# Kernel optimization log

Hardware: AMD Instinct MI355X
Metric: run time of the kernel (lower is better)

The kernel has to match this reference:

```python
import jax, jax.numpy as jnp
import numpy as np

N_NODES = 100000
N_EDGES = 3200000
BN_EPS = 1e-5


def setup_inputs() -> dict:
    key = jax.random.key(0)
    ks = jax.random.split(key, 16)
    return {
        "x": jax.random.normal(ks[0], (N_NODES, 2), jnp.float32),
        "eq_labels": jax.random.randint(ks[1], (N_NODES,), 0, 32, jnp.int32),
        "edge_index": jax.random.randint(ks[2], (2, N_EDGES), 0, N_NODES, jnp.int32),
        "eq_emb": jax.random.normal(ks[3], (32, 8), jnp.float32),
        "W1_0": jax.random.normal(ks[4], (10, 64), jnp.float32) * 0.3,
        "b1_0": jnp.zeros((64,), jnp.float32),
        "W2_0": jax.random.normal(ks[5], (64, 64), jnp.float32) * 0.12,
        "b2_0": jnp.zeros((64,), jnp.float32),
        "eps_0": jnp.zeros((), jnp.float32),
        "gamma_0": jnp.ones((64,), jnp.float32),
        "beta_0": jnp.zeros((64,), jnp.float32),
        "W1_s": jax.random.normal(ks[6], (2, 64, 64), jnp.float32) * 0.12,
        "b1_s": jnp.zeros((2, 64), jnp.float32),
        "W2_s": jax.random.normal(ks[7], (2, 64, 64), jnp.float32) * 0.12,
        "b2_s": jnp.zeros((2, 64), jnp.float32),
        "eps_s": jnp.zeros((2,), jnp.float32),
        "gamma_s": jnp.ones((2, 64), jnp.float32),
        "beta_s": jnp.zeros((2, 64), jnp.float32),
        "Wf": jax.random.normal(ks[8], (64, 1), jnp.float32) * 0.12,
        "bf": jnp.zeros((1,), jnp.float32),
    }


def _gin_bn_relu(h, src, dst, W1, b1, W2, b2, eps, gamma, beta):
    # GINConv: (1+eps)*x_i + sum_{j->i} x_j, then 2-layer ReLU MLP, then BN, ReLU
    agg = jax.ops.segment_sum(h[src], dst, num_segments=N_NODES)
    h = (1.0 + eps) * h + agg
    h = jax.nn.relu(h @ W1 + b1)
    h = jax.nn.relu(h @ W2 + b2)
    mu = jnp.mean(h, axis=0)
    var = jnp.var(h, axis=0)
    h = (h - mu) * jax.lax.rsqrt(var + BN_EPS) * gamma + beta
    return jax.nn.relu(h)


def reference(x, eq_labels, edge_index, eq_emb, W1_0, b1_0, W2_0, b2_0, eps_0,
              gamma_0, beta_0, W1_s, b1_s, W2_s, b2_s, eps_s, gamma_s, beta_s,
              Wf, bf):
    src, dst = edge_index[0], edge_index[1]
    h = jnp.concatenate([x, eq_emb[eq_labels]], axis=-1)  # [N, 10]
    h = _gin_bn_relu(h, src, dst, W1_0, b1_0, W2_0, b2_0, eps_0, gamma_0, beta_0)
    for i in range(2):
        h = _gin_bn_relu(h, src, dst, W1_s[i], b1_s[i], W2_s[i], b2_s[i],
                         eps_s[i], gamma_s[i], beta_s[i])
    return (h @ Wf + bf).squeeze(-1)  # [N]
```

## Files before the change

### kernel.cpp

```cpp
#include <hip/hip_runtime.h>

#define N_NODES 100000
#define N_EDGES 3200000
#define BN_EPS 1e-5f

#define BLK_NODES 128
#define NBLK 782
#define CHUNK 16384
#define NW ((N_EDGES + CHUNK - 1) / CHUNK)
#define BCAP 4480
#define CUR_PAD 16
#define NSLICE 32

typedef unsigned int uint;
typedef unsigned short ushort;
typedef _Float16 half_t;
typedef __attribute__((ext_vector_type(8))) _Float16 h8v;
typedef __attribute__((ext_vector_type(4))) float f4v;

__device__ inline float bf_lo(uint u) { return __uint_as_float(u << 16); }
__device__ inline float bf_hi(uint u) { return __uint_as_float(u & 0xffff0000u); }
__device__ inline float h_lo(uint u) {
    union { ushort s; half_t h; } r; r.s = (ushort)(u & 0xffffu); return (float)r.h;
}
__device__ inline float h_hi(uint u) {
    union { ushort s; half_t h; } r; r.s = (ushort)(u >> 16); return (float)r.h;
}
__device__ inline ushort f2bf(float a) {
    uint ua = __float_as_uint(a); ua += 0x7fffu + ((ua >> 16) & 1u);
    return (ushort)(ua >> 16);
}
__device__ inline ushort f2h(float a) {
    union { half_t h; ushort u; } r;
    r.h = (half_t)a;
    return r.u;
}
__device__ inline uint packh2(float a, float b) {
    return (uint)f2h(a) | ((uint)f2h(b) << 16);
}
__device__ inline h8v loadH(const ushort* p) {
    union { uint4 q; h8v f; } r;
    r.q = *(const uint4*)p;
    return r.f;
}
__device__ inline h8v loadHh(const half_t* p) {
    union { uint4 q; h8v f; } r;
    r.q = *(const uint4*)p;
    return r.f;
}
__device__ inline f4v mfma16(h8v a, h8v b, f4v c) {
    return __builtin_amdgcn_mfma_f32_16x16x32_f16(a, b, c, 0, 0, 0);
}

#define FETCH_COLS(rr, st, dg, mx, wv, wv2)                                   \
    {                                                                         \
        int _r = (rr);                                                        \
        st = __shfl(myStart, 2 * _r + hl, 64);                                \
        dg = __shfl(myDeg, 2 * _r + hl, 64);                                  \
        int _dA = __shfl(myDeg, 2 * _r, 64);                                  \
        int _dB = __shfl(myDeg, 2 * _r + 1, 64);                              \
        mx = max(_dA, _dB);                                                   \
        int _e1 = min(l5, dg - 1); _e1 = _e1 < 0 ? 0 : _e1;                   \
        int _e2 = min(32 + l5, dg - 1); _e2 = _e2 < 0 ? 0 : _e2;              \
        wv = col[st + _e1];                                                   \
        wv2 = col[st + _e2];                                                  \
    }

__global__ __launch_bounds__(256) void k_h0(const float* __restrict__ x,
                                            const int* __restrict__ lab,
                                            const float* __restrict__ emb,
                                            ushort* __restrict__ h0,
                                            const float* __restrict__ W1_0,
                                            const float* __restrict__ W2_0,
                                            const float* __restrict__ W1_s,
                                            const float* __restrict__ W2_s,
                                            ushort* __restrict__ W0t,
                                            ushort* __restrict__ W20t,
                                            ushort* __restrict__ Wst, int n) {
    int i = blockIdx.x * blockDim.x + threadIdx.x;
    if (i < n) {
        float v[16];
        v[0] = x[2 * i];
        v[1] = x[2 * i + 1];
        int L = lab[i];
#pragma unroll
        for (int k = 0; k < 8; k++) v[2 + k] = emb[L * 8 + k];
#pragma unroll
        for (int k = 10; k < 16; k++) v[k] = 0.f;
        uint o8[8];
#pragma unroll
        for (int k = 0; k < 8; k++) o8[k] = packh2(v[2 * k], v[2 * k + 1]);
        uint4* o = (uint4*)(h0 + (size_t)i * 16);
        o[0] = uint4{o8[0], o8[1], o8[2], o8[3]};
        o[1] = uint4{o8[4], o8[5], o8[6], o8[7]};
    }
    if (blockIdx.x == 0) {
        int t = threadIdx.x;
        for (int j = t; j < 64 * 32; j += 256) {
            int nn = j >> 5, k = j & 31;
            W0t[j] = (k < 10) ? f2h(W1_0[k * 64 + nn]) : (ushort)0;
        }
        for (int j = t; j < 4096; j += 256) {
            int nn = j >> 6, k = j & 63;
            W20t[j] = f2h(W2_0[k * 64 + nn]);
        }
        for (int l = 0; l < 2; l++) {
            const float* w1 = W1_s + l * 4096;
            const float* w2 = W2_s + l * 4096;
            for (int j = t; j < 4096; j += 256) {
                int nn = j >> 6, k = j & 63;
                Wst[l * 8192 + j] = f2h(w1[k * 64 + nn]);
                Wst[l * 8192 + 4096 + j] = f2h(w2[k * 64 + nn]);
            }
        }
    }
}

__global__ __launch_bounds__(256) void k_fill(const int* __restrict__ src,
                                              const int* __restrict__ dst,
                                              int* __restrict__ gcur,
                                              int* __restrict__ bucket) {
    __shared__ int cnt[NBLK];
    __shared__ int off[NBLK];
    int t = threadIdx.x;
    for (int b = t; b < NBLK; b += 256) cnt[b] = 0;
    __syncthreads();
    int my0 = blockIdx.x * CHUNK + t * 64;
    for (int k = 0; k < 64; k += 4) {
        int e = my0 + k;
        if (e + 3 < N_EDGES) {
            int4 d4 = *(const int4*)(dst + e);
            atomicAdd(&cnt[d4.x >> 7], 1);
            atomicAdd(&cnt[d4.y >> 7], 1);
            atomicAdd(&cnt[d4.z >> 7], 1);
            atomicAdd(&cnt[d4.w >> 7], 1);
        } else {
#pragma unroll
            for (int kk = 0; kk < 4; kk++) {
                int ee = e + kk;
                if (ee < N_EDGES) atomicAdd(&cnt[dst[ee] >> 7], 1);
            }
        }
    }
    __syncthreads();
    for (int b = t; b < NBLK; b += 256) {
        int c = cnt[b];
        off[b] = (c > 0) ? atomicAdd(&gcur[b * CUR_PAD], c) : 0;
    }
    __syncthreads();
    for (int k = 0; k < 64; k += 4) {
        int e = my0 + k;
        if (e + 3 < N_EDGES) {
            int4 d4 = *(const int4*)(dst + e);
            int4 s4 = *(const int4*)(src + e);
            int dd[4] = {d4.x, d4.y, d4.z, d4.w};
            int ss[4] = {s4.x, s4.y, s4.z, s4.w};
#pragma unroll
            for (int kk = 0; kk < 4; kk++) {
                int b = dd[kk] >> 7;
                int p = atomicAdd(&off[b], 1);
                if (p < BCAP)
                    bucket[(size_t)b * BCAP + p] = ((dd[kk] & 127) << 17) | ss[kk];
            }
        } else {
#pragma unroll
            for (int kk = 0; kk < 4; kk++) {
                int ee = e + kk;
                if (ee < N_EDGES) {
                    int d = dst[ee], s = src[ee];
                    int b = d >> 7;
                    int p = atomicAdd(&off[b], 1);
                    if (p < BCAP)
                        bucket[(size_t)b * BCAP + p] = ((d & 127) << 17) | s;
                }
            }
        }
    }
}

__global__ __launch_bounds__(256) void k_sort(const int* __restrict__ gcur,
                                              const int* __restrict__ bucket,
                                              int* __restrict__ col2,
                                              int2* __restrict__ nodeoff, int n) {
    __shared__ int cnt[BLK_NODES];
    __shared__ int scn[BLK_NODES];
    __shared__ int cur[BLK_NODES];
    int t = threadIdx.x;
    int blk = blockIdx.x;
    if (t < BLK_NODES) cnt[t] = 0;
    __syncthreads();
    int cc = min(gcur[blk * CUR_PAD], BCAP);
    const int* bb = bucket + (size_t)blk * BCAP;
    for (int i = t; i < cc; i += 256) atomicAdd(&cnt[bb[i] >> 17], 1);
    __syncthreads();
    if (t < BLK_NODES) scn[t] = cnt[t];
    __syncthreads();
#pragma unroll
    for (int off = 1; off < BLK_NODES; off <<= 1) {
        int v = (t >= off && t < BLK_NODES) ? scn[t - off] : 0;
        __syncthreads();
        if (t < BLK_NODES) scn[t] += v;
        __syncthreads();
    }
    if (t < BLK_NODES) {
        int start = scn[t] - cnt[t];
        cur[t] = start;
        int node = blk * BLK_NODES + t;
        if (node < n) nodeoff[node] = int2{blk * BCAP + start, cnt[t]};
    }
    __syncthreads();
    int* out = col2 + (size_t)blk * BCAP;
    for (int i = t; i < cc; i += 256) {
        int w = bb[i];
        int p = atomicAdd(&cur[w >> 17], 1);
        out[p] = w & 0x1FFFF;
    }
}

__global__ __launch_bounds__(256, 4) void k_layer0M(const ushort* __restrict__ h0,
                                                    const int2* __restrict__ nodeoff,
                                                    const int* __restrict__ col,
                                                    const float* __restrict__ epsp,
                                                    const ushort* __restrict__ W0t,
                                                    const float* __restrict__ b1,
                                                    const ushort* __restrict__ W20t,
                                                    const float* __restrict__ b2,
                                                    ushort* __restrict__ hraw,
                                                    float* __restrict__ part_out) {
    __shared__ half_t buf[4][16][72];
    int t = threadIdx.x, w = t >> 6, lane = t & 63;
    int base = blockIdx.x * 64 + w * 16;
    float ep = 1.f + *epsp;
    int hl = lane >> 5, l5 = lane & 31;
    int q = l5 & 3, g = l5 >> 2;
    const uint* hb = (const uint*)h0;

    int nj = base + (lane & 15);
    int2 no2 = nodeoff[nj];
    bool njv = nj < N_NODES;
    int myStart = njv ? no2.x : 0;
    int myDeg = njv ? no2.y : 0;

    int stC, dgC, mxC, wvC, wv2C;
    int stN, dgN, mxN, wvN, wv2N;
    FETCH_COLS(0, stC, dgC, mxC, wvC, wv2C);
    FETCH_COLS(1, stN, dgN, mxN, wvN, wv2N);
    uint2 rowsC[4];
#pragma unroll
    for (int i = 0; i < 4; i++) {
        int ix = __shfl(wvC, (hl << 5) + g + 8 * i, 64);
        rowsC[i] = *(const uint2*)(hb + (size_t)ix * 8 + q * 2);
    }

    for (int r = 0; r < 8; r++) {
        int stNN, dgNN, mxNN, wvNN, wv2NN;
        FETCH_COLS(min(r + 2, 7), stNN, dgNN, mxNN, wvNN, wv2NN);
        uint2 rows2[4];
#pragma unroll
        for (int i = 0; i < 4; i++) {
            int ix = __shfl(wv2C, (hl << 5) + g + 8 * i, 64);
            rows2[i] = *(const uint2*)(hb + (size_t)ix * 8 + q * 2);
        }
        int deg = dgC;
        float ac[4] = {0.f, 0.f, 0.f, 0.f};
#pragma unroll
        for (int i = 0; i < 4; i++) {
            float m = (g + 8 * i < deg) ? 1.f : 0.f;
            ac[0] = fmaf(m, h_lo(rowsC[i].x), ac[0]);
            ac[1] = fmaf(m, h_hi(rowsC[i].x), ac[1]);
            ac[2] = fmaf(m, h_lo(rowsC[i].y), ac[2]);
            ac[3] = fmaf(m, h_hi(rowsC[i].y), ac[3]);
        }
        uint2 rowsN[4];
#pragma unroll
        for (int i = 0; i < 4; i++) {
            int ix = __shfl(wvN, (hl << 5) + g + 8 * i, 64);
            rowsN[i] = *(const uint2*)(hb + (size_t)ix * 8 + q * 2);
        }
#pragma unroll
        for (int i = 0; i < 4; i++) {
            float m = (32 + g + 8 * i < deg) ? 1.f : 0.f;
            ac[0] = fmaf(m, h_lo(rows2[i].x), ac[0]);
            ac[1] = fmaf(m, h_hi(rows2[i].x), ac[1]);
            ac[2] = fmaf(m, h_lo(rows2[i].y), ac[2]);
            ac[3] = fmaf(m, h_hi(rows2[i].y), ac[3]);
        }
        if (mxC > 64) {
            for (int e = 64 + g; e < deg; e += 8) {
                uint2 v = *(const uint2*)(hb + (size_t)col[stC + e] * 8 + q * 2);
                ac[0] += h_lo(v.x); ac[1] += h_hi(v.x);
                ac[2] += h_lo(v.y); ac[3] += h_hi(v.y);
            }
        }
#pragma unroll
        for (int o = 4; o < 32; o <<= 1) {
#pragma unroll
            for (int k = 0; k < 4; k++) ac[k] += __shfl_xor(ac[k], o, 64);
        }
        int node = base + 2 * r + hl;
        bool valid = node < N_NODES;
        int nodeC = valid ? node : 0;
        float vm = valid ? ep : 0.f;
        uint2 sv = *(const uint2*)(hb + (size_t)nodeC * 8 + q * 2);
        ac[0] = fmaf(vm, h_lo(sv.x), ac[0]);
        ac[1] = fmaf(vm, h_hi(sv.x), ac[1]);
        ac[2] = fmaf(vm, h_lo(sv.y), ac[2]);
        ac[3] = fmaf(vm, h_hi(sv.y), ac[3]);
        if (!valid) { ac[0] = ac[1] = ac[2] = ac[3] = 0.f; }
        if (g == 0) {
            int nl = 2 * r + hl;
            *(uint2*)&buf[w][nl][q * 4] = uint2{packh2(ac[0], ac[1]), packh2(ac[2], ac[3])};
            *(uint2*)&buf[w][nl][16 + q * 4] = uint2{0u, 0u};
        }
        stC = stN; dgC = dgN; mxC = mxN; wvC = wvN; wv2C = wv2N;
        stN = stNN; dgN = dgNN; mxN = mxNN; wvN = wvNN; wv2N = wv2NN;
#pragma unroll
        for (int i = 0; i < 4; i++) rowsC[i] = rowsN[i];
    }
    int mr = lane & 15, kq = lane >> 4, nc = lane & 15;
    h8v A0 = loadHh(&buf[w][mr][kq * 8]);
#pragma unroll
    for (int nt = 0; nt < 4; nt++) {
        float bb = b1[nt * 16 + nc];
        f4v c = {bb, bb, bb, bb};
        c = mfma16(A0, loadH(W0t + (nt * 16 + nc) * 32 + kq * 8), c);
#pragma unroll
        for (int r2 = 0; r2 < 4; r2++)
            buf[w][kq * 4 + r2][nt * 16 + nc] = (half_t)fmaxf(c[r2], 0.f);
    }
    h8v P0 = loadHh(&buf[w][mr][kq * 8]);
    h8v P1 = loadHh(&buf[w][mr][32 + kq * 8]);
    float sA[4], sB[4];
#pragma unroll
    for (int nt = 0; nt < 4; nt++) { sA[nt] = 0.f; sB[nt] = 0.f; }
#pragma unroll
    for (int nt = 0; nt < 4; nt++) {
        float bb = b2[nt * 16 + nc];
        f4v c = {bb, bb, bb, bb};
        c = mfma16(P0, loadH(W20t + (nt * 16 + nc) * 64 + kq * 8), c);
        c = mfma16(P1, loadH(W20t + (nt * 16 + nc) * 64 + 32 + kq * 8), c);
#pragma unroll
        for (int r2 = 0; r2 < 4; r2++) {
            int node = base + kq * 4 + r2;
            float vv = fmaxf(c[r2], 0.f);
            if (node < N_NODES) {
                sA[nt] += vv;
                sB[nt] = fmaf(vv, vv, sB[nt]);
                hraw[(size_t)node * 64 + nt * 16 + nc] = f2h(vv);
            }
        }
    }
#pragma unroll
    for (int o = 16; o < 64; o <<= 1) {
#pragma unroll
        for (int nt = 0; nt < 4; nt++) {
            sA[nt] += __shfl_xor(sA[nt], o, 64);
            sB[nt] += __shfl_xor(sB[nt], o, 64);
        }
    }
    if (kq == 0) {
        float* pp = part_out + (blockIdx.x & (NSLICE - 1)) * 128;
#pragma unroll
        for (int nt = 0; nt < 4; nt++) {
            atomicAdd(&pp[nt * 16 + nc], sA[nt]);
            atomicAdd(&pp[64 + nt * 16 + nc], sB[nt]);
        }
    }
}

__global__ __launch_bounds__(256) void k_act(const ushort* __restrict__ hraw,
                                             const float* __restrict__ part,
                                             const float* __restrict__ gamma,
                                             const float* __restrict__ beta,
                                             ushort* __restrict__ act, float invn) {
    __shared__ float st[128];
    __shared__ float sc[64], sh[64];
    int t = threadIdx.x;
    if (t < 128) {
        float S = 0.f;
#pragma unroll 8
        for (int s = 0; s < NSLICE; s++) S += part[s * 128 + t];
        st[t] = S;
    }
    __syncthreads();
    if (t < 64) {
        float mu = st[t] * invn;
        float var = fmaxf(st[64 + t] * invn - mu * mu, 0.f);
        float s = gamma[t] * rsqrtf(var + BN_EPS);
        sc[t] = s;
        sh[t] = beta[t] - mu * s;
    }
    __syncthreads();
    int base = (blockIdx.x * 256 + t) * 4;
    int f0 = base & 63;
    uint2 hv = *(const uint2*)(hraw + base);
    float a0 = fmaxf(fmaf(h_lo(hv.x), sc[f0 + 0], sh[f0 + 0]), 0.f);
    float a1 = fmaxf(fmaf(h_hi(hv.x), sc[f0 + 1], sh[f0 + 1]), 0.f);
    float a2 = fmaxf(fmaf(h_lo(hv.y), sc[f0 + 2], sh[f0 + 2]), 0.f);
    float a3 = fmaxf(fmaf(h_hi(hv.y), sc[f0 + 3], sh[f0 + 3]), 0.f);
    uint2 o;
    o.x = (uint)f2bf(a0) | ((uint)f2bf(a1) << 16);
    o.y = (uint)f2bf(a2) | ((uint)f2bf(a3) << 16);
    *(uint2*)(act + base) = o;
}

__global__ __launch_bounds__(256, 4) void k_layerM(const uint* __restrict__ actin,
                                                   const int2* __restrict__ nodeoff,
                                                   const int* __restrict__ col,
                                                   const float* __restrict__ epsp,
                                                   const ushort* __restrict__ W1t,
                                                   const float* __restrict__ b1,
                                                   const ushort* __restrict__ W2t,
                                                   const float* __restrict__ b2,
                                                   ushort* __restrict__ hraw,
                                                   float* __restrict__ part_out) {
    __shared__ half_t buf[4][16][72];
    int t = threadIdx.x, w = t >> 6, lane = t & 63;
    int base = blockIdx.x * 64 + w * 16;
    float ep = 1.f + *epsp;
    int hl = lane >> 5, l5 = lane & 31;
    int q = l5 & 7, g = l5 >> 3;
    const uint4* hb4 = (const uint4*)actin;

    int nj = base + (lane & 15);
    int2 no2 = nodeoff[nj];
    bool njv = nj < N_NODES;
    int myStart = njv ? no2.x : 0;
    int myDeg = njv ? no2.y : 0;

    int stC, dgC, mxC, wvC, wv2C;
    int stN, dgN, mxN, wvN, wv2N;
    FETCH_COLS(0, stC, dgC, mxC, wvC, wv2C);
    FETCH_COLS(1, stN, dgN, mxN, wvN, wv2N);
    uint4 rowsC[8];
#pragma unroll
    for (int i = 0; i < 8; i++) {
        int ix = __shfl(wvC, (hl << 5) + g + 4 * i, 64);
        rowsC[i] = hb4[(size_t)ix * 8 + q];
    }

    for (int r = 0; r < 8; r++) {
        int stNN, dgNN, mxNN, wvNN, wv2NN;
        FETCH_COLS(min(r + 2, 7), stNN, dgNN, mxNN, wvNN, wv2NN);
        uint4 rows2[8];
#pragma unroll
        for (int i = 0; i < 8; i++) {
            int ix = __shfl(wv2C, (hl << 5) + g + 4 * i, 64);
            rows2[i] = hb4[(size_t)ix * 8 + q];
        }
        int deg = dgC;
        float acc[8];
#pragma unroll
        for (int k = 0; k < 8; k++) acc[k] = 0.f;
        auto procm = [&](uint4 v, float m) {
            acc[0] = fmaf(m, bf_lo(v.x), acc[0]);
            acc[1] = fmaf(m, bf_hi(v.x), acc[1]);
            acc[2] = fmaf(m, bf_lo(v.y), acc[2]);
            acc[3] = fmaf(m, bf_hi(v.y), acc[3]);
            acc[4] = fmaf(m, bf_lo(v.z), acc[4]);
            acc[5] = fmaf(m, bf_hi(v.z), acc[5]);
            acc[6] = fmaf(m, bf_lo(v.w), acc[6]);
            acc[7] = fmaf(m, bf_hi(v.w), acc[7]);
        };
#pragma unroll
        for (int i = 0; i < 8; i++) procm(rowsC[i], (g + 4 * i < deg) ? 1.f : 0.f);
        uint4 rowsN[8];
#pragma unroll
        for (int i = 0; i < 8; i++) {
            int ix = __shfl(wvN, (hl << 5) + g + 4 * i, 64);
            rowsN[i] = hb4[(size_t)ix * 8 + q];
        }
#pragma unroll
        for (int i = 0; i < 8; i++) procm(rows2[i], (32 + g + 4 * i < deg) ? 1.f : 0.f);
        if (mxC > 64) {
            for (int e = 64 + g; e < deg; e += 4)
                procm(hb4[(size_t)col[stC + e] * 8 + q], 1.f);
        }
#pragma unroll
        for (int o = 8; o < 32; o <<= 1) {
#pragma unroll
            for (int k = 0; k < 8; k++) acc[k] += __shfl_xor(acc[k], o, 64);
        }
        int node = base + 2 * r + hl;
        bool valid = node < N_NODES;
        int nodeC = valid ? node : 0;
        float vm = valid ? ep : 0.f;
        uint4 v = hb4[(size_t)nodeC * 8 + q];
        acc[0] = fmaf(vm, bf_lo(v.x), acc[0]);
        acc[1] = fmaf(vm, bf_hi(v.x), acc[1]);
        acc[2] = fmaf(vm, bf_lo(v.y), acc[2]);
        acc[3] = fmaf(vm, bf_hi(v.y), acc[3]);
        acc[4] = fmaf(vm, bf_lo(v.z), acc[4]);
        acc[5] = fmaf(vm, bf_hi(v.z), acc[5]);
        acc[6] = fmaf(vm, bf_lo(v.w), acc[6]);
        acc[7] = fmaf(vm, bf_hi(v.w), acc[7]);
        if (!valid) {
#pragma unroll
            for (int k = 0; k < 8; k++) acc[k] = 0.f;
        }
        if (g == 0) {
            int nl = 2 * r + hl;
            *(uint2*)&buf[w][nl][q * 8 + 0] = uint2{packh2(acc[0], acc[1]), packh2(acc[2], acc[3])};
            *(uint2*)&buf[w][nl][q * 8 + 4] = uint2{packh2(acc[4], acc[5]), packh2(acc[6], acc[7])};
        }
        stC = stN; dgC = dgN; mxC = mxN; wvC = wvN; wv2C = wv2N;
        stN = stNN; dgN = dgNN; mxN = mxNN; wvN = wvNN; wv2N = wv2NN;
#pragma unroll
        for (int i = 0; i < 8; i++) rowsC[i] = rowsN[i];
    }
    int mr = lane & 15, kq = lane >> 4, nc = lane & 15;
    h8v A0 = loadHh(&buf[w][mr][kq * 8]);
    h8v A1 = loadHh(&buf[w][mr][32 + kq * 8]);
#pragma unroll
    for (int nt = 0; nt < 4; nt++) {
        float bb = b1[nt * 16 + nc];
        f4v c = {bb, bb, bb, bb};
        c = mfma16(A0, loadH(W1t + (nt * 16 + nc) * 64 + kq * 8), c);
        c = mfma16(A1, loadH(W1t + (nt * 16 + nc) * 64 + 32 + kq * 8), c);
#pragma unroll
        for (int r2 = 0; r2 < 4; r2++)
            buf[w][kq * 4 + r2][nt * 16 + nc] = (half_t)fmaxf(c[r2], 0.f);
    }
    h8v P0 = loadHh(&buf[w][mr][kq * 8]);
    h8v P1 = loadHh(&buf[w][mr][32 + kq * 8]);
    float sA[4], sB[4];
#pragma unroll
    for (int nt = 0; nt < 4; nt++) { sA[nt] = 0.f; sB[nt] = 0.f; }
#pragma unroll
    for (int nt = 0; nt < 4; nt++) {
        float bb = b2[nt * 16 + nc];
        f4v c = {bb, bb, bb, bb};
        c = mfma16(P0, loadH(W2t + (nt * 16 + nc) * 64 + kq * 8), c);
        c = mfma16(P1, loadH(W2t + (nt * 16 + nc) * 64 + 32 + kq * 8), c);
#pragma unroll
        for (int r2 = 0; r2 < 4; r2++) {
            int node = base + kq * 4 + r2;
            float vv = fmaxf(c[r2], 0.f);
            if (node < N_NODES) {
                sA[nt] += vv;
                sB[nt] = fmaf(vv, vv, sB[nt]);
                hraw[(size_t)node * 64 + nt * 16 + nc] = f2h(vv);
            }
        }
    }
#pragma unroll
    for (int o = 16; o < 64; o <<= 1) {
#pragma unroll
        for (int nt = 0; nt < 4; nt++) {
            sA[nt] += __shfl_xor(sA[nt], o, 64);
            sB[nt] += __shfl_xor(sB[nt], o, 64);
        }
    }
    if (kq == 0) {
        float* pp = part_out + (blockIdx.x & (NSLICE - 1)) * 128;
#pragma unroll
        for (int nt = 0; nt < 4; nt++) {
            atomicAdd(&pp[nt * 16 + nc], sA[nt]);
            atomicAdd(&pp[64 + nt * 16 + nc], sB[nt]);
        }
    }
}

__global__ __launch_bounds__(256) void k_out(const ushort* __restrict__ hraw,
                                             const float* __restrict__ part,
                                             const float* __restrict__ gamma,
                                             const float* __restrict__ beta,
                                             const float* __restrict__ Wf,
                                             const float* __restrict__ bfp,
                                             float* __restrict__ out, int n,
                                             float invn) {
    __shared__ float st[128];
    __shared__ float sc[64], sh[64];
    int t = threadIdx.x;
    if (t < 128) {
        float S = 0.f;
#pragma unroll 8
        for (int s = 0; s < NSLICE; s++) S += part[s * 128 + t];
        st[t] = S;
    }
    __syncthreads();
    if (t < 64) {
        float mu = st[t] * invn;
        float var = fmaxf(st[64 + t] * invn - mu * mu, 0.f);
        float s = gamma[t] * rsqrtf(var + BN_EPS);
        sc[t] = s;
        sh[t] = beta[t] - mu * s;
    }
    __syncthreads();
    int i = blockIdx.x * blockDim.x + threadIdx.x;
    if (i >= n) return;
    float acc = *bfp;
    const uint2* h2 = (const uint2*)(hraw + (size_t)i * 64);
#pragma unroll
    for (int qq = 0; qq < 16; qq++) {
        uint2 v = h2[qq];
        int j = qq * 4;
        acc = fmaf(fmaxf(fmaf(h_lo(v.x), sc[j + 0], sh[j + 0]), 0.f), Wf[j + 0], acc);
        acc = fmaf(fmaxf(fmaf(h_hi(v.x), sc[j + 1], sh[j + 1]), 0.f), Wf[j + 1], acc);
        acc = fmaf(fmaxf(fmaf(h_lo(v.y), sc[j + 2], sh[j + 2]), 0.f), Wf[j + 2], acc);
        acc = fmaf(fmaxf(fmaf(h_hi(v.y), sc[j + 3], sh[j + 3]), 0.f), Wf[j + 3], acc);
    }
    out[i] = acc;
}

extern "C" void kernel_launch(void* const* d_in, const int* in_sizes, int n_in,
                              void* d_out, int out_size, void* d_ws, size_t ws_size,
                              hipStream_t stream) {
    const float* x      = (const float*)d_in[0];
    const int*   lab    = (const int*)d_in[1];
    const int*   edge   = (const int*)d_in[2];
    const float* emb    = (const float*)d_in[3];
    const float* W1_0   = (const float*)d_in[4];
    const float* b1_0   = (const float*)d_in[5];
    const float* W2_0   = (const float*)d_in[6];
    const float* b2_0   = (const float*)d_in[7];
    const float* eps_0  = (const float*)d_in[8];
    const float* gamma_0= (const float*)d_in[9];
    const float* beta_0 = (const float*)d_in[10];
    const float* W1_s   = (const float*)d_in[11];
    const float* b1_s   = (const float*)d_in[12];
    const float* W2_s   = (const float*)d_in[13];
    const float* b2_s   = (const float*)d_in[14];
    const float* eps_s  = (const float*)d_in[15];
    const float* gamma_s= (const float*)d_in[16];
    const float* beta_s = (const float*)d_in[17];
    const float* Wf     = (const float*)d_in[18];
    const float* bf     = (const float*)d_in[19];

    const int N = N_NODES, E = N_EDGES;
    const int* srcp = edge;
    const int* dstp = edge + E;

    char* p = (char*)d_ws;
    auto alloc = [&](size_t bytes) {
        void* r = (void*)p;
        p += (bytes + 255) & ~(size_t)255;
        return r;
    };
    int* bucket  = (int*)alloc((size_t)NBLK * BCAP * 4);
    int* col2    = (int*)alloc((size_t)NBLK * BCAP * 4);
    int* gcur    = (int*)alloc((size_t)NBLK * CUR_PAD * 4);
    int* nodeoff = (int*)alloc((size_t)(N + 64) * 8);
    ushort* hraw = (ushort*)alloc((size_t)N * 64 * 2);
    ushort* act  = (ushort*)alloc((size_t)N * 64 * 2);
    ushort* h0   = (ushort*)alloc((size_t)N * 16 * 2);
    float* parts = (float*)alloc(3 * NSLICE * 128 * 4);
    ushort* W0t  = (ushort*)alloc(64 * 32 * 2);
    ushort* W20t = (ushort*)alloc(4096 * 2);
    ushort* Wst  = (ushort*)alloc(2 * 8192 * 2);

    hipMemsetAsync(gcur, 0, (size_t)NBLK * CUR_PAD * 4, stream);
    hipMemsetAsync(parts, 0, 3 * NSLICE * 128 * 4, stream);

    const int TB = 256;
    const int gN = (N + TB - 1) / TB;
    const int gM = (N + 63) / 64;
    const int gA = N * 64 / 1024;
    const float invn = 1.0f / (float)N;

    k_h0<<<gN, TB, 0, stream>>>(x, lab, emb, h0, W1_0, W2_0, W1_s, W2_s,
                                W0t, W20t, Wst, N);
    k_fill<<<NW, TB, 0, stream>>>(srcp, dstp, gcur, bucket);
    k_sort<<<NBLK, TB, 0, stream>>>(gcur, bucket, col2, (int2*)nodeoff, N);

    k_layer0M<<<gM, TB, 0, stream>>>(h0, (const int2*)nodeoff, col2, eps_0, W0t,
                                     b1_0, W20t, b2_0, hraw,
                                     parts + 0 * NSLICE * 128);
    k_act<<<gA, TB, 0, stream>>>(hraw, parts + 0 * NSLICE * 128, gamma_0, beta_0,
                                 act, invn);

    k_layerM<<<gM, TB, 0, stream>>>((const uint*)act, (const int2*)nodeoff, col2,
                                    eps_s + 0, Wst + 0 * 8192, b1_s + 0 * 64,
                                    Wst + 0 * 8192 + 4096, b2_s + 0 * 64,
                                    hraw, parts + 1 * NSLICE * 128);
    k_act<<<gA, TB, 0, stream>>>(hraw, parts + 1 * NSLICE * 128, gamma_s + 0 * 64,
                                 beta_s + 0 * 64, act, invn);

    k_layerM<<<gM, TB, 0, stream>>>((const uint*)act, (const int2*)nodeoff, col2,
                                    eps_s + 1, Wst + 1 * 8192, b1_s + 1 * 64,
                                    Wst + 1 * 8192 + 4096, b2_s + 1 * 64,
                                    hraw, parts + 2 * NSLICE * 128);

    k_out<<<gN, TB, 0, stream>>>(hraw, parts + 2 * NSLICE * 128,
                                 gamma_s + 1 * 64, beta_s + 1 * 64, Wf, bf,
                                 (float*)d_out, N, invn);
}
```

Baseline: 384.7 us.

## Aggregate neighbors via MFMA over contiguous edge ranges in 64-wide layers

The 64-feature layer kernel replaces per-node shuffle-and-sum neighbor gathering with a per-wave sweep over the contiguous CSR edge range of its 16 nodes. Each 32-edge chunk of gathered rows is staged in swizzled shared memory and reduced by an MFMA against a 0/1 membership matrix, so the adds run on matrix cores and the loads become fully coalesced 64-wide row reads. The activation storage switches from bf16 to fp16 to match the new half-precision operands. The layer-0 gather skips loads when a node has no neighbors and drops the cross-iteration row prefetch. This adds LDS traffic and relies on sorted contiguous edges and padded nodeoff, which is now zeroed.

New measurement: 405.6 us. 1.05x slower.

```diff
diff --git a/kernel.cpp b/kernel.cpp
--- a/kernel.cpp
+++ b/kernel.cpp
@@ -245,51 +245,49 @@
     int stN, dgN, mxN, wvN, wv2N;
     FETCH_COLS(0, stC, dgC, mxC, wvC, wv2C);
     FETCH_COLS(1, stN, dgN, mxN, wvN, wv2N);
-    uint2 rowsC[4];
-#pragma unroll
-    for (int i = 0; i < 4; i++) {
-        int ix = __shfl(wvC, (hl << 5) + g + 8 * i, 64);
-        rowsC[i] = *(const uint2*)(hb + (size_t)ix * 8 + q * 2);
-    }
 
     for (int r = 0; r < 8; r++) {
         int stNN, dgNN, mxNN, wvNN, wv2NN;
         FETCH_COLS(min(r + 2, 7), stNN, dgNN, mxNN, wvNN, wv2NN);
-        uint2 rows2[4];
-#pragma unroll
-        for (int i = 0; i < 4; i++) {
-            int ix = __shfl(wv2C, (hl << 5) + g + 8 * i, 64);
-            rows2[i] = *(const uint2*)(hb + (size_t)ix * 8 + q * 2);
-        }
-        int deg = dgC;
+        int deg = dgC, mx = mxC;
         float ac[4] = {0.f, 0.f, 0.f, 0.f};
-#pragma unroll
-        for (int i = 0; i < 4; i++) {
-            float m = (g + 8 * i < deg) ? 1.f : 0.f;
-            ac[0] = fmaf(m, h_lo(rowsC[i].x), ac[0]);
-            ac[1] = fmaf(m, h_hi(rowsC[i].x), ac[1]);
-            ac[2] = fmaf(m, h_lo(rowsC[i].y), ac[2]);
-            ac[3] = fmaf(m, h_hi(rowsC[i].y), ac[3]);
-        }
-        uint2 rowsN[4];
-#pragma unroll
-        for (int i = 0; i < 4; i++) {
-            int ix = __shfl(wvN, (hl << 5) + g + 8 * i, 64);
-            rowsN[i] = *(const uint2*)(hb + (size_t)ix * 8 + q * 2);
-        }
-#pragma unroll
-        for (int i = 0; i < 4; i++) {
-            float m = (32 + g + 8 * i < deg) ? 1.f : 0.f;
-            ac[0] = fmaf(m, h_lo(rows2[i].x), ac[0]);
-            ac[1] = fmaf(m, h_hi(rows2[i].x), ac[1]);
-            ac[2] = fmaf(m, h_lo(rows2[i].y), ac[2]);
-            ac[3] = fmaf(m, h_hi(rows2[i].y), ac[3]);
-        }
-        if (mxC > 64) {
-            for (int e = 64 + g; e < deg; e += 8) {
-                uint2 v = *(const uint2*)(hb + (size_t)col[stC + e] * 8 + q * 2);
-                ac[0] += h_lo(v.x); ac[1] += h_hi(v.x);
-                ac[2] += h_lo(v.y); ac[3] += h_hi(v.y);
+        if (mx > 0) {
+            int idx[4];
+#pragma unroll
+            for (int i = 0; i < 4; i++) idx[i] = __shfl(wvC, (hl << 5) + g + 8 * i, 64);
+            uint2 rows[4];
+#pragma unroll
+            for (int i = 0; i < 4; i++)
+                rows[i] = *(const uint2*)(hb + (size_t)idx[i] * 8 + q * 2);
+#pragma unroll
+            for (int i = 0; i < 4; i++) {
+                float m = (g + 8 * i < deg) ? 1.f : 0.f;
+                ac[0] = fmaf(m, h_lo(rows[i].x), ac[0]);
+                ac[1] = fmaf(m, h_hi(rows[i].x), ac[1]);
+                ac[2] = fmaf(m, h_lo(rows[i].y), ac[2]);
+                ac[3] = fmaf(m, h_hi(rows[i].y), ac[3]);
+            }
+            if (mx > 32) {
+                int idx2[4];
+#pragma unroll
+                for (int i = 0; i < 4; i++) idx2[i] = __shfl(wv2C, (hl << 5) + g + 8 * i, 64);
+                uint2 rows2[4];
+#pragma unroll
+                for (int i = 0; i < 4; i++)
+                    rows2[i] = *(const uint2*)(hb + (size_t)idx2[i] * 8 + q * 2);
+#pragma unroll
+                for (int i = 0; i < 4; i++) {
+                    float m = (32 + g + 8 * i < deg) ? 1.f : 0.f;
+                    ac[0] = fmaf(m, h_lo(rows2[i].x), ac[0]);
+                    ac[1] = fmaf(m, h_hi(rows2[i].x), ac[1]);
+                    ac[2] = fmaf(m, h_lo(rows2[i].y), ac[2]);
+                    ac[3] = fmaf(m, h_hi(rows2[i].y), ac[3]);
+                }
+                for (int e = 64 + g; e < deg; e += 8) {
+                    uint2 v = *(const uint2*)(hb + (size_t)col[stC + e] * 8 + q * 2);
+                    ac[0] += h_lo(v.x); ac[1] += h_hi(v.x);
+                    ac[2] += h_lo(v.y); ac[3] += h_hi(v.y);
+                }
             }
         }
 #pragma unroll
@@ -314,8 +312,6 @@
         }
         stC = stN; dgC = dgN; mxC = mxN; wvC = wvN; wv2C = wv2N;
         stN = stNN; dgN = dgNN; mxN = mxNN; wvN = wvNN; wv2N = wv2NN;
-#pragma unroll
-        for (int i = 0; i < 4; i++) rowsC[i] = rowsN[i];
     }
     int mr = lane & 15, kq = lane >> 4, nc = lane & 15;
     h8v A0 = loadHh(&buf[w][mr][kq * 8]);
@@ -399,8 +395,8 @@
     float a2 = fmaxf(fmaf(h_lo(hv.y), sc[f0 + 2], sh[f0 + 2]), 0.f);
     float a3 = fmaxf(fmaf(h_hi(hv.y), sc[f0 + 3], sh[f0 + 3]), 0.f);
     uint2 o;
-    o.x = (uint)f2bf(a0) | ((uint)f2bf(a1) << 16);
-    o.y = (uint)f2bf(a2) | ((uint)f2bf(a3) << 16);
+    o.x = packh2(a0, a1);
+    o.y = packh2(a2, a3);
     *(uint2*)(act + base) = o;
 }
 
@@ -414,101 +410,90 @@
                                                    const float* __restrict__ b2,
                                                    ushort* __restrict__ hraw,
                                                    float* __restrict__ part_out) {
+    __shared__ ushort stg[4][2048];
     __shared__ half_t buf[4][16][72];
     int t = threadIdx.x, w = t >> 6, lane = t & 63;
-    int base = blockIdx.x * 64 + w * 16;
+    int wbase = blockIdx.x * 64 + w * 16;
     float ep = 1.f + *epsp;
-    int hl = lane >> 5, l5 = lane & 31;
-    int q = l5 & 7, g = l5 >> 3;
-    const uint4* hb4 = (const uint4*)actin;
-
-    int nj = base + (lane & 15);
+    int nc = lane & 15, kq = lane >> 4;
+    const ushort* au = (const ushort*)actin;
+
+    int nj = wbase + nc;
     int2 no2 = nodeoff[nj];
     bool njv = nj < N_NODES;
-    int myStart = njv ? no2.x : 0;
-    int myDeg = njv ? no2.y : 0;
-
-    int stC, dgC, mxC, wvC, wv2C;
-    int stN, dgN, mxN, wvN, wv2N;
-    FETCH_COLS(0, stC, dgC, mxC, wvC, wv2C);
-    FETCH_COLS(1, stN, dgN, mxN, wvN, wv2N);
-    uint4 rowsC[8];
-#pragma unroll
-    for (int i = 0; i < 8; i++) {
-        int ix = __shfl(wvC, (hl << 5) + g + 4 * i, 64);
-        rowsC[i] = hb4[(size_t)ix * 8 + q];
-    }
-
-    for (int r = 0; r < 8; r++) {
-        int stNN, dgNN, mxNN, wvNN, wv2NN;
-        FETCH_COLS(min(r + 2, 7), stNN, dgNN, mxNN, wvNN, wv2NN);
-        uint4 rows2[8];
-#pragma unroll
-        for (int i = 0; i < 8; i++) {
-            int ix = __shfl(wv2C, (hl << 5) + g + 4 * i, 64);
-            rows2[i] = hb4[(size_t)ix * 8 + q];
-        }
-        int deg = dgC;
-        float acc[8];
-#pragma unroll
-        for (int k = 0; k < 8; k++) acc[k] = 0.f;
-        auto procm = [&](uint4 v, float m) {
-            acc[0] = fmaf(m, bf_lo(v.x), acc[0]);
-            acc[1] = fmaf(m, bf_hi(v.x), acc[1]);
-            acc[2] = fmaf(m, bf_lo(v.y), acc[2]);
-            acc[3] = fmaf(m, bf_hi(v.y), acc[3]);
-            acc[4] = fmaf(m, bf_lo(v.z), acc[4]);
-            acc[5] = fmaf(m, bf_hi(v.z), acc[5]);
-            acc[6] = fmaf(m, bf_lo(v.w), acc[6]);
-            acc[7] = fmaf(m, bf_hi(v.w), acc[7]);
-        };
-#pragma unroll
-        for (int i = 0; i < 8; i++) procm(rowsC[i], (g + 4 * i < deg) ? 1.f : 0.f);
-        uint4 rowsN[8];
-#pragma unroll
-        for (int i = 0; i < 8; i++) {
-            int ix = __shfl(wvN, (hl << 5) + g + 4 * i, 64);
-            rowsN[i] = hb4[(size_t)ix * 8 + q];
-        }
-#pragma unroll
-        for (int i = 0; i < 8; i++) procm(rows2[i], (32 + g + 4 * i < deg) ? 1.f : 0.f);
-        if (mxC > 64) {
-            for (int e = 64 + g; e < deg; e += 4)
-                procm(hb4[(size_t)col[stC + e] * 8 + q], 1.f);
-        }
-#pragma unroll
-        for (int o = 8; o < 32; o <<= 1) {
-#pragma unroll
-            for (int k = 0; k < 8; k++) acc[k] += __shfl_xor(acc[k], o, 64);
-        }
-        int node = base + 2 * r + hl;
-        bool valid = node < N_NODES;
-        int nodeC = valid ? node : 0;
-        float vm = valid ? ep : 0.f;
-        uint4 v = hb4[(size_t)nodeC * 8 + q];
-        acc[0] = fmaf(vm, bf_lo(v.x), acc[0]);
-        acc[1] = fmaf(vm, bf_hi(v.x), acc[1]);
-        acc[2] = fmaf(vm, bf_lo(v.y), acc[2]);
-        acc[3] = fmaf(vm, bf_hi(v.y), acc[3]);
-        acc[4] = fmaf(vm, bf_lo(v.z), acc[4]);
-        acc[5] = fmaf(vm, bf_hi(v.z), acc[5]);
-        acc[6] = fmaf(vm, bf_lo(v.w), acc[6]);
-        acc[7] = fmaf(vm, bf_hi(v.w), acc[7]);
-        if (!valid) {
-#pragma unroll
-            for (int k = 0; k < 8; k++) acc[k] = 0.f;
-        }
-        if (g == 0) {
-            int nl = 2 * r + hl;
-            *(uint2*)&buf[w][nl][q * 8 + 0] = uint2{packh2(acc[0], acc[1]), packh2(acc[2], acc[3])};
-            *(uint2*)&buf[w][nl][q * 8 + 4] = uint2{packh2(acc[4], acc[5]), packh2(acc[6], acc[7])};
-        }
-        stC = stN; dgC = dgN; mxC = mxN; wvC = wvN; wv2C = wv2N;
-        stN = stNN; dgN = dgNN; mxN = mxNN; wvN = wvNN; wv2N = wv2NN;
-#pragma unroll
-        for (int i = 0; i < 8; i++) rowsC[i] = rowsN[i];
-    }
-    int mr = lane & 15, kq = lane >> 4, nc = lane & 15;
+    int sm = njv ? no2.x : 0;
+    int dm = njv ? no2.y : 0;
+    int se = sm + dm;
+
+    int e0 = __shfl(sm, 0, 64);
+    int eEnd = __shfl(se, 15, 64);
+    e0 = max(0, min(e0, NBLK * BCAP - 1));
+    int T = max(eEnd - e0, 0);
+    int eLast = min(e0 + max(T - 1, 0), NBLK * BCAP - 1);
+    int C = min((max(T, 1) + 31) >> 5, (BCAP + 31) >> 5);
+
+    f4v acc[4];
+#pragma unroll
+    for (int nt = 0; nt < 4; nt++) {
+#pragma unroll
+        for (int r = 0; r < 4; r++) {
+            int nd = wbase + kq * 4 + r;
+            float vm = (nd < N_NODES) ? ep : 0.f;
+            int ndc = (nd < N_NODES) ? nd : 0;
+            acc[nt][r] = vm * h_lo(au[(size_t)ndc * 64 + nt * 16 + nc]);
+        }
+    }
+
+    int s5 = lane & 31, hh = lane >> 5;
+    int kqs = s5 >> 3;
+    int kk = (s5 & 24) | ((s5 & 7) ^ kqs);
+    int baseX = kq * 144 + (nc >> 3) * 512 + (nc & 7) * 2;
+    char* tb = (char*)&stg[w][0];
+
+    int colv = min(col[min(e0 + s5, eLast)] & 0x1FFFF, N_NODES - 1);
+
+    for (int j = 0; j < C; j++) {
+        int cvk = __shfl(colv, kk, 64);
+        const ushort* gs = au + (size_t)cvk * 64 + hh * 8;
+        uint4 rv0 = *(const uint4*)(gs);
+        uint4 rv1 = *(const uint4*)(gs + 16);
+        uint4 rv2 = *(const uint4*)(gs + 32);
+        uint4 rv3 = *(const uint4*)(gs + 48);
+        int ci = min(e0 + (j + 1) * 32 + s5, eLast);
+        int colvN = min(col[ci] & 0x1FFFF, N_NODES - 1);
+        char* lw = tb + lane * 16;
+        *(uint4*)(lw) = rv0;
+        *(uint4*)(lw + 1024) = rv1;
+        *(uint4*)(lw + 2048) = rv2;
+        *(uint4*)(lw + 3072) = rv3;
+        int eb = e0 + j * 32 + kq * 8;
+        union { uint u[4]; h8v v; } aw;
+#pragma unroll
+        for (int p = 0; p < 4; p++) {
+            int ea = eb + 2 * p;
+            uint lo = (ea >= sm && ea < se) ? 0x3C00u : 0u;
+            uint hi = (ea + 1 >= sm && ea + 1 < se) ? 0x3C000000u : 0u;
+            aw.u[p] = lo | hi;
+        }
+#pragma unroll
+        for (int nt = 0; nt < 4; nt++) {
+            union { ushort u[8]; h8v v; } bf;
+#pragma unroll
+            for (int jj = 0; jj < 8; jj++)
+                bf.u[jj] = *(const ushort*)(tb + nt * 1024 + (baseX ^ (jj << 4)));
+            acc[nt] = mfma16(aw.v, bf.v, acc[nt]);
+        }
+        colv = colvN;
+    }
+
+#pragma unroll
+    for (int nt = 0; nt < 4; nt++) {
+#pragma unroll
+        for (int r2 = 0; r2 < 4; r2++)
+            buf[w][kq * 4 + r2][nt * 16 + nc] = (half_t)acc[nt][r2];
+    }
+
+    int mr = lane & 15;
     h8v A0 = loadHh(&buf[w][mr][kq * 8]);
     h8v A1 = loadHh(&buf[w][mr][32 + kq * 8]);
 #pragma unroll
@@ -534,7 +519,7 @@
         c = mfma16(P1, loadH(W2t + (nt * 16 + nc) * 64 + 32 + kq * 8), c);
 #pragma unroll
         for (int r2 = 0; r2 < 4; r2++) {
-            int node = base + kq * 4 + r2;
+            int node = wbase + kq * 4 + r2;
             float vv = fmaxf(c[r2], 0.f);
             if (node < N_NODES) {
                 sA[nt] += vv;
@@ -651,6 +636,7 @@
 
     hipMemsetAsync(gcur, 0, (size_t)NBLK * CUR_PAD * 4, stream);
     hipMemsetAsync(parts, 0, 3 * NSLICE * 128 * 4, stream);
+    hipMemsetAsync(nodeoff + 2 * (size_t)N, 0, 64 * 8, stream);
 
     const int TB = 256;
     const int gN = (N + TB - 1) / TB;
```

## Replace software-pipelined neighbor gathers with degree-gated loads and fp16 activations

Applied to the files above, without the earlier changes.

The gather loops in the layer kernels drop the cross-iteration register prefetch of neighbor rows. They now issue loads only when the pair's max degree is nonzero, and load the second 32-edge batch only when it exceeds 32. This cuts wasted gathers for low-degree nodes and lowers register pressure, at the cost of less latency hiding across iterations. The activation buffer also switches from bf16 to fp16, both when written in k_act and when read in the layer kernels. The padding area of nodeoff is now zeroed so the tail lanes read defined values.

After: 379.8 us. Within noise of the previous version (-1.3%).

```diff
diff --git a/kernel.cpp b/kernel.cpp
--- a/kernel.cpp
+++ b/kernel.cpp
@@ -245,51 +245,49 @@
     int stN, dgN, mxN, wvN, wv2N;
     FETCH_COLS(0, stC, dgC, mxC, wvC, wv2C);
     FETCH_COLS(1, stN, dgN, mxN, wvN, wv2N);
-    uint2 rowsC[4];
-#pragma unroll
-    for (int i = 0; i < 4; i++) {
-        int ix = __shfl(wvC, (hl << 5) + g + 8 * i, 64);
-        rowsC[i] = *(const uint2*)(hb + (size_t)ix * 8 + q * 2);
-    }
 
     for (int r = 0; r < 8; r++) {
         int stNN, dgNN, mxNN, wvNN, wv2NN;
         FETCH_COLS(min(r + 2, 7), stNN, dgNN, mxNN, wvNN, wv2NN);
-        uint2 rows2[4];
-#pragma unroll
-        for (int i = 0; i < 4; i++) {
-            int ix = __shfl(wv2C, (hl << 5) + g + 8 * i, 64);
-            rows2[i] = *(const uint2*)(hb + (size_t)ix * 8 + q * 2);
-        }
-        int deg = dgC;
+        int deg = dgC, mx = mxC;
         float ac[4] = {0.f, 0.f, 0.f, 0.f};
-#pragma unroll
-        for (int i = 0; i < 4; i++) {
-            float m = (g + 8 * i < deg) ? 1.f : 0.f;
-            ac[0] = fmaf(m, h_lo(rowsC[i].x), ac[0]);
-            ac[1] = fmaf(m, h_hi(rowsC[i].x), ac[1]);
-            ac[2] = fmaf(m, h_lo(rowsC[i].y), ac[2]);
-            ac[3] = fmaf(m, h_hi(rowsC[i].y), ac[3]);
-        }
-        uint2 rowsN[4];
-#pragma unroll
-        for (int i = 0; i < 4; i++) {
-            int ix = __shfl(wvN, (hl << 5) + g + 8 * i, 64);
-            rowsN[i] = *(const uint2*)(hb + (size_t)ix * 8 + q * 2);
-        }
-#pragma unroll
-        for (int i = 0; i < 4; i++) {
-            float m = (32 + g + 8 * i < deg) ? 1.f : 0.f;
-            ac[0] = fmaf(m, h_lo(rows2[i].x), ac[0]);
-            ac[1] = fmaf(m, h_hi(rows2[i].x), ac[1]);
-            ac[2] = fmaf(m, h_lo(rows2[i].y), ac[2]);
-            ac[3] = fmaf(m, h_hi(rows2[i].y), ac[3]);
-        }
-        if (mxC > 64) {
-            for (int e = 64 + g; e < deg; e += 8) {
-                uint2 v = *(const uint2*)(hb + (size_t)col[stC + e] * 8 + q * 2);
-                ac[0] += h_lo(v.x); ac[1] += h_hi(v.x);
-                ac[2] += h_lo(v.y); ac[3] += h_hi(v.y);
+        if (mx > 0) {
+            int idx[4];
+#pragma unroll
+            for (int i = 0; i < 4; i++) idx[i] = __shfl(wvC, (hl << 5) + g + 8 * i, 64);
+            uint2 rows[4];
+#pragma unroll
+            for (int i = 0; i < 4; i++)
+                rows[i] = *(const uint2*)(hb + (size_t)idx[i] * 8 + q * 2);
+#pragma unroll
+            for (int i = 0; i < 4; i++) {
+                float m = (g + 8 * i < deg) ? 1.f : 0.f;
+                ac[0] = fmaf(m, h_lo(rows[i].x), ac[0]);
+                ac[1] = fmaf(m, h_hi(rows[i].x), ac[1]);
+                ac[2] = fmaf(m, h_lo(rows[i].y), ac[2]);
+                ac[3] = fmaf(m, h_hi(rows[i].y), ac[3]);
+            }
+            if (mx > 32) {
+                int idx2[4];
+#pragma unroll
+                for (int i = 0; i < 4; i++) idx2[i] = __shfl(wv2C, (hl << 5) + g + 8 * i, 64);
+                uint2 rows2[4];
+#pragma unroll
+                for (int i = 0; i < 4; i++)
+                    rows2[i] = *(const uint2*)(hb + (size_t)idx2[i] * 8 + q * 2);
+#pragma unroll
+                for (int i = 0; i < 4; i++) {
+                    float m = (32 + g + 8 * i < deg) ? 1.f : 0.f;
+                    ac[0] = fmaf(m, h_lo(rows2[i].x), ac[0]);
+                    ac[1] = fmaf(m, h_hi(rows2[i].x), ac[1]);
+                    ac[2] = fmaf(m, h_lo(rows2[i].y), ac[2]);
+                    ac[3] = fmaf(m, h_hi(rows2[i].y), ac[3]);
+                }
+                for (int e = 64 + g; e < deg; e += 8) {
+                    uint2 v = *(const uint2*)(hb + (size_t)col[stC + e] * 8 + q * 2);
+                    ac[0] += h_lo(v.x); ac[1] += h_hi(v.x);
+                    ac[2] += h_lo(v.y); ac[3] += h_hi(v.y);
+                }
             }
         }
 #pragma unroll
@@ -314,8 +312,6 @@
         }
         stC = stN; dgC = dgN; mxC = mxN; wvC = wvN; wv2C = wv2N;
         stN = stNN; dgN = dgNN; mxN = mxNN; wvN = wvNN; wv2N = wv2NN;
-#pragma unroll
-        for (int i = 0; i < 4; i++) rowsC[i] = rowsN[i];
     }
     int mr = lane & 15, kq = lane >> 4, nc = lane & 15;
     h8v A0 = loadHh(&buf[w][mr][kq * 8]);
@@ -399,8 +395,8 @@
     float a2 = fmaxf(fmaf(h_lo(hv.y), sc[f0 + 2], sh[f0 + 2]), 0.f);
     float a3 = fmaxf(fmaf(h_hi(hv.y), sc[f0 + 3], sh[f0 + 3]), 0.f);
     uint2 o;
-    o.x = (uint)f2bf(a0) | ((uint)f2bf(a1) << 16);
-    o.y = (uint)f2bf(a2) | ((uint)f2bf(a3) << 16);
+    o.x = packh2(a0, a1);
+    o.y = packh2(a2, a3);
     *(uint2*)(act + base) = o;
 }
 
@@ -432,49 +428,45 @@
     int stN, dgN, mxN, wvN, wv2N;
     FETCH_COLS(0, stC, dgC, mxC, wvC, wv2C);
     FETCH_COLS(1, stN, dgN, mxN, wvN, wv2N);
-    uint4 rowsC[8];
-#pragma unroll
-    for (int i = 0; i < 8; i++) {
-        int ix = __shfl(wvC, (hl << 5) + g + 4 * i, 64);
-        rowsC[i] = hb4[(size_t)ix * 8 + q];
-    }
 
     for (int r = 0; r < 8; r++) {
         int stNN, dgNN, mxNN, wvNN, wv2NN;
         FETCH_COLS(min(r + 2, 7), stNN, dgNN, mxNN, wvNN, wv2NN);
-        uint4 rows2[8];
-#pragma unroll
-        for (int i = 0; i < 8; i++) {
-            int ix = __shfl(wv2C, (hl << 5) + g + 4 * i, 64);
-            rows2[i] = hb4[(size_t)ix * 8 + q];
-        }
         int deg = dgC;
         float acc[8];
 #pragma unroll
         for (int k = 0; k < 8; k++) acc[k] = 0.f;
         auto procm = [&](uint4 v, float m) {
-            acc[0] = fmaf(m, bf_lo(v.x), acc[0]);
-            acc[1] = fmaf(m, bf_hi(v.x), acc[1]);
-            acc[2] = fmaf(m, bf_lo(v.y), acc[2]);
-            acc[3] = fmaf(m, bf_hi(v.y), acc[3]);
-            acc[4] = fmaf(m, bf_lo(v.z), acc[4]);
-            acc[5] = fmaf(m, bf_hi(v.z), acc[5]);
-            acc[6] = fmaf(m, bf_lo(v.w), acc[6]);
-            acc[7] = fmaf(m, bf_hi(v.w), acc[7]);
+            acc[0] = fmaf(m, h_lo(v.x), acc[0]);
+            acc[1] = fmaf(m, h_hi(v.x), acc[1]);
+            acc[2] = fmaf(m, h_lo(v.y), acc[2]);
+            acc[3] = fmaf(m, h_hi(v.y), acc[3]);
+            acc[4] = fmaf(m, h_lo(v.z), acc[4]);
+            acc[5] = fmaf(m, h_hi(v.z), acc[5]);
+            acc[6] = fmaf(m, h_lo(v.w), acc[6]);
+            acc[7] = fmaf(m, h_hi(v.w), acc[7]);
         };
-#pragma unroll
-        for (int i = 0; i < 8; i++) procm(rowsC[i], (g + 4 * i < deg) ? 1.f : 0.f);
-        uint4 rowsN[8];
-#pragma unroll
-        for (int i = 0; i < 8; i++) {
-            int ix = __shfl(wvN, (hl << 5) + g + 4 * i, 64);
-            rowsN[i] = hb4[(size_t)ix * 8 + q];
-        }
-#pragma unroll
-        for (int i = 0; i < 8; i++) procm(rows2[i], (32 + g + 4 * i < deg) ? 1.f : 0.f);
-        if (mxC > 64) {
-            for (int e = 64 + g; e < deg; e += 4)
-                procm(hb4[(size_t)col[stC + e] * 8 + q], 1.f);
+        if (mxC > 0) {
+            int idx[8];
+#pragma unroll
+            for (int i = 0; i < 8; i++) idx[i] = __shfl(wvC, (hl << 5) + g + 4 * i, 64);
+            uint4 rows[8];
+#pragma unroll
+            for (int i = 0; i < 8; i++) rows[i] = hb4[(size_t)idx[i] * 8 + q];
+#pragma unroll
+            for (int i = 0; i < 8; i++) procm(rows[i], (g + 4 * i < deg) ? 1.f : 0.f);
+            if (mxC > 32) {
+                int idx2[8];
+#pragma unroll
+                for (int i = 0; i < 8; i++) idx2[i] = __shfl(wv2C, (hl << 5) + g + 4 * i, 64);
+                uint4 rows2[8];
+#pragma unroll
+                for (int i = 0; i < 8; i++) rows2[i] = hb4[(size_t)idx2[i] * 8 + q];
+#pragma unroll
+                for (int i = 0; i < 8; i++) procm(rows2[i], (32 + g + 4 * i < deg) ? 1.f : 0.f);
+                for (int e = 64 + g; e < deg; e += 4)
+                    procm(hb4[(size_t)col[stC + e] * 8 + q], 1.f);
+            }
         }
 #pragma unroll
         for (int o = 8; o < 32; o <<= 1) {
@@ -486,14 +478,14 @@
         int nodeC = valid ? node : 0;
         float vm = valid ? ep : 0.f;
         uint4 v = hb4[(size_t)nodeC * 8 + q];
-        acc[0] = fmaf(vm, bf_lo(v.x), acc[0]);
-        acc[1] = fmaf(vm, bf_hi(v.x), acc[1]);
-        acc[2] = fmaf(vm, bf_lo(v.y), acc[2]);
-        acc[3] = fmaf(vm, bf_hi(v.y), acc[3]);
-        acc[4] = fmaf(vm, bf_lo(v.z), acc[4]);
-        acc[5] = fmaf(vm, bf_hi(v.z), acc[5]);
-        acc[6] = fmaf(vm, bf_lo(v.w), acc[6]);
-        acc[7] = fmaf(vm, bf_hi(v.w), acc[7]);
+        acc[0] = fmaf(vm, h_lo(v.x), acc[0]);
+        acc[1] = fmaf(vm, h_hi(v.x), acc[1]);
+        acc[2] = fmaf(vm, h_lo(v.y), acc[2]);
+        acc[3] = fmaf(vm, h_hi(v.y), acc[3]);
+        acc[4] = fmaf(vm, h_lo(v.z), acc[4]);
+        acc[5] = fmaf(vm, h_hi(v.z), acc[5]);
+        acc[6] = fmaf(vm, h_lo(v.w), acc[6]);
+        acc[7] = fmaf(vm, h_hi(v.w), acc[7]);
         if (!valid) {
 #pragma unroll
             for (int k = 0; k < 8; k++) acc[k] = 0.f;
@@ -505,8 +497,6 @@
         }
         stC = stN; dgC = dgN; mxC = mxN; wvC = wvN; wv2C = wv2N;
         stN = stNN; dgN = dgNN; mxN = mxNN; wvN = wvNN; wv2N = wv2NN;
-#pragma unroll
-        for (int i = 0; i < 8; i++) rowsC[i] = rowsN[i];
     }
     int mr = lane & 15, kq = lane >> 4, nc = lane & 15;
     h8v A0 = loadHh(&buf[w][mr][kq * 8]);
@@ -651,6 +641,7 @@
 
     hipMemsetAsync(gcur, 0, (size_t)NBLK * CUR_PAD * 4, stream);
     hipMemsetAsync(parts, 0, 3 * NSLICE * 128 * 4, stream);
+    hipMemsetAsync(nodeoff + 2 * (size_t)N, 0, 64 * 8, stream);
 
     const int TB = 256;
     const int gN = (N + TB - 1) / TB;
```
